# Performance work log

Measured on AMD Instinct MI355X. Metric: run time of the kernel, lower is better.

Reference implementation:

```python
import jax, jax.numpy as jnp
import numpy as np
import math

D_MODEL = 768
N_HEADS = 6
HD = D_MODEL // N_HEADS  # 128
RANK = D_MODEL // 4      # 192
B, T = 128, 256


def _rope_tables(T, dim):
    # matches torch: inv = 1/10000**(arange(0,dim,2)/dim); emb = cat([outer(t,inv)]*2, -1)
    inv = 1.0 / (10000.0 ** (jnp.arange(0, dim, 2, dtype=jnp.float32) / dim))
    t = jnp.arange(T, dtype=jnp.float32)
    freqs = jnp.outer(t, inv)                       # [T, dim/2]
    emb = jnp.concatenate([freqs, freqs], axis=-1)  # [T, dim]
    return jnp.cos(emb), jnp.sin(emb)               # each [T, dim]


def _rot(x):
    h = x.shape[-1] // 2
    return jnp.concatenate([-x[..., h:], x[..., :h]], axis=-1)


def setup_inputs() -> dict:
    key = jax.random.key(0)
    ks = jax.random.split(key, 8)
    s_in = 1.0 / math.sqrt(D_MODEL)
    s_r = 1.0 / math.sqrt(RANK)
    inp = {
        'x': jax.random.normal(ks[0], (B, T, D_MODEL), dtype=jnp.float32),
        'qA': jax.random.normal(ks[1], (D_MODEL, RANK), dtype=jnp.float32) * s_in,
        'qB': jax.random.normal(ks[2], (RANK, D_MODEL), dtype=jnp.float32) * s_r,
        'kA': jax.random.normal(ks[3], (D_MODEL, RANK), dtype=jnp.float32) * s_in,
        'kB': jax.random.normal(ks[4], (RANK, D_MODEL), dtype=jnp.float32) * s_r,
        'vA': jax.random.normal(ks[5], (D_MODEL, RANK), dtype=jnp.float32) * s_in,
        'vB': jax.random.normal(ks[6], (RANK, D_MODEL), dtype=jnp.float32) * s_r,
        'o_w': jax.random.normal(ks[7], (D_MODEL, D_MODEL), dtype=jnp.float32) * s_in,
    }
    return inp


def reference(x, qA, qB, kA, kB, vA, vB, o_w):
    Bb, Tt, _ = x.shape
    # low-rank projections: in -> rank -> out, then split heads [B, H, T, hd]
    def proj(A, W):
        h = (x @ A) @ W
        return h.reshape(Bb, Tt, N_HEADS, HD).transpose(0, 2, 1, 3)
    q = proj(qA, qB)
    k = proj(kA, kB)
    v = proj(vA, vB)
    cos, sin = _rope_tables(Tt, HD)  # [T, hd], broadcast over B, H
    q = q * cos + _rot(q) * sin
    k = k * cos + _rot(k) * sin
    att = jnp.einsum('bhqd,bhkd->bhqk', q, k) / math.sqrt(HD)
    causal = jnp.tril(jnp.ones((Tt, Tt), dtype=bool))
    att = jnp.where(causal, att, -jnp.inf)
    att = jax.nn.softmax(att, axis=-1)
    out = jnp.einsum('bhqk,bhkd->bhqd', att, v)          # [B, H, T, hd]
    out = out.transpose(0, 2, 1, 3).reshape(Bb, Tt, D_MODEL)
    return out @ o_w
```

## Files before the change

kernel.cpp:

```cpp
#include <hip/hip_runtime.h>
#include <hip/hip_bf16.h>
#include <stdint.h>

typedef __attribute__((ext_vector_type(8))) short s16x8;
typedef __attribute__((ext_vector_type(4))) float f32x4;

#define D_MODEL 768
#define N_HEADS 6
#define HD 128
#define RANK 192
#define TT 256
#define NROW 32768
#define QKV_LD 2304
#define NK 12
#define QSCL 0.08838834764831845f

__device__ inline short f2bf(float f) {
  union { float f; unsigned u; } x; x.f = f;
  unsigned r = x.u + 0x7fffu + ((x.u >> 16) & 1u);
  return (short)(r >> 16);
}
__device__ inline float bf2f(short v) {
  union { unsigned u; float f; } x; x.u = ((unsigned)(unsigned short)v) << 16;
  return x.f;
}
__device__ inline void gload_lds16(const void* g, void* lds) {
  __builtin_amdgcn_global_load_lds(
      (const __attribute__((address_space(1))) unsigned int*)g,
      (__attribute__((address_space(3))) unsigned int*)lds, 16, 0, 0);
}

#define BAR()    asm volatile("s_barrier" ::: "memory")
#define LGKM0()  asm volatile("s_waitcnt lgkmcnt(0)" ::: "memory")
#define WAITVM4() asm volatile("s_waitcnt vmcnt(4)" ::: "memory")
#define WAITVM0() asm volatile("s_waitcnt vmcnt(0)" ::: "memory")

__global__ void k_tables(float* __restrict__ cosT, float* __restrict__ sinT) {
  int tid = blockIdx.x * 256 + threadIdx.x;
  int t = tid >> 6, i = tid & 63;
  float inv = powf(10000.0f, -(float)i / 64.0f);
  float ang = (float)t * inv;
  cosT[tid] = cosf(ang);
  sinT[tid] = sinf(ang);
}

__global__ void k_castx(const float* __restrict__ x, short* __restrict__ xb) {
  int t = blockIdx.x * 256 + threadIdx.x;
  const float4* xp = (const float4*)x;
  float4 a = xp[t * 2], b = xp[t * 2 + 1];
  s16x8 o;
  o[0] = f2bf(a.x); o[1] = f2bf(a.y); o[2] = f2bf(a.z); o[3] = f2bf(a.w);
  o[4] = f2bf(b.x); o[5] = f2bf(b.y); o[6] = f2bf(b.z); o[7] = f2bf(b.w);
  *(s16x8*)(xb + (size_t)t * 8) = o;
}

__global__ void k_makew(const float* __restrict__ qA, const float* __restrict__ qB,
                        const float* __restrict__ kA, const float* __restrict__ kB,
                        const float* __restrict__ vA, const float* __restrict__ vB,
                        short* __restrict__ WT) {
  int g = blockIdx.x * 256 + threadIdx.x;
  int n4 = g % 576, kkb = g / 576;
  int part = n4 / 192, nnb = (n4 % 192) * 4;
  const float* A = (part == 0) ? qA : (part == 1) ? kA : vA;
  const float* Bm = (part == 0) ? qB : (part == 1) ? kB : vB;
  float acc[4][4] = {};
  for (int r0 = 0; r0 < RANK; r0 += 4) {
    float4 a4[4], b4[4];
#pragma unroll
    for (int q = 0; q < 4; ++q)
      a4[q] = *(const float4*)&A[(kkb + q * 192) * RANK + r0];
#pragma unroll
    for (int i = 0; i < 4; ++i)
      b4[i] = *(const float4*)&Bm[(r0 + i) * 768 + nnb];
#pragma unroll
    for (int q = 0; q < 4; ++q) {
      const float* aq = (const float*)&a4[q];
#pragma unroll
      for (int i = 0; i < 4; ++i) {
        const float* bi = (const float*)&b4[i];
#pragma unroll
        for (int jn = 0; jn < 4; ++jn)
          acc[q][jn] += aq[i] * bi[jn];
      }
    }
  }
#pragma unroll
  for (int q = 0; q < 4; ++q)
#pragma unroll
    for (int jn = 0; jn < 4; ++jn)
      WT[(size_t)(part * 768 + nnb + jn) * 768 + kkb + q * 192] = f2bf(acc[q][jn]);
}

__global__ void k_wot(const float* __restrict__ ow, short* __restrict__ WT) {
  int g = blockIdx.x * 256 + threadIdx.x;
  int n = g % 768, kk = g / 768;
  WT[(size_t)(2304 + n) * 768 + kk] = f2bf(ow[(size_t)kk * 768 + n]);
}

__device__ inline s16x8 rdfrag(const short* hbase, int rowbyte, int ksl4x, int swz) {
  return *(const s16x8*)((const char*)hbase + rowbyte + (((ksl4x) ^ (swz)) << 4));
}

template <bool OUTBF>
__global__ __launch_bounds__(512, 2) void k_gemm8(const short* __restrict__ A,
                                                  const short* __restrict__ Bt,
                                                  void* __restrict__ Cv, int ldc) {
  extern __shared__ short lds[];
  const int tid = threadIdx.x;
  const int wid = tid >> 6, lane = tid & 63;
  const int l15 = lane & 15, l4 = lane >> 4;
  const int wr = wid >> 2, wc = wid & 3;
  const int swz = l15 & 7;
  const int bid = blockIdx.y * 128 + blockIdx.x;
  const int nper = gridDim.y;
  const int xcd = bid & 7, loc = bid >> 3;
  const int mq = loc / nper;
  const int mt = xcd * 16 + mq;
  const int nt = loc - mq * nper;
  const long mbase = (long)mt * 256;
  const long nbase = (long)nt * 256;

  const int hb0 = wid * 2048 + lane * 16;
  const int hb1 = hb0 + 1024;
  const int r0 = hb0 >> 7, c0 = ((hb0 >> 4) & 7) ^ (r0 & 7);
  const int r1 = hb1 >> 7, c1 = ((hb1 >> 4) & 7) ^ (r1 & 7);
  const int off0 = r0 * 768 + c0 * 8;
  const int off1 = r1 * 768 + c1 * 8;

#define STAGE(G, rowoff, kt, ldsS) do {                                        \
    gload_lds16((G) + (size_t)(rowoff) * 768 + (kt) * 64 + off0,               \
                (char*)(ldsS) + wid * 2048);                                   \
    gload_lds16((G) + (size_t)(rowoff) * 768 + (kt) * 64 + off1,               \
                (char*)(ldsS) + wid * 2048 + 1024);                            \
  } while (0)

#define LDSA(buf, half) (lds + ((buf) * 2 + (half)) * 8192)
#define LDSB(buf, half) (lds + 32768 + ((buf) * 2 + (half)) * 8192)

  f32x4 acc[8][4] = {};

  STAGE(A,  mbase,       0, LDSA(0, 0));
  STAGE(Bt, nbase,       0, LDSB(0, 0));
  STAGE(A,  mbase + 128, 0, LDSA(0, 1));
  STAGE(Bt, nbase + 128, 0, LDSB(0, 1));
  STAGE(A,  mbase,       1, LDSA(1, 0));
  STAGE(Bt, nbase,       1, LDSB(1, 0));
  WAITVM4();
  BAR();

  s16x8 a03[4][2], a47[4][2], b01[2][2], b23[2][2];

#pragma unroll
  for (int kt = 0; kt < NK; ++kt) {
    const int buf = kt & 1, nbuf = buf ^ 1;
    const short* Ab = LDSA(buf, wr);
    const short* Bb = LDSB(buf, (wc >> 1));
    const int browbase = (wc & 1) * 64 * 128;

#pragma unroll
    for (int mf = 0; mf < 4; ++mf)
#pragma unroll
      for (int ks = 0; ks < 2; ++ks)
        a03[mf][ks] = rdfrag(Ab, (mf * 16 + l15) * 128, ks * 4 + l4, swz);
#pragma unroll
    for (int nf = 0; nf < 2; ++nf)
#pragma unroll
      for (int ks = 0; ks < 2; ++ks)
        b01[nf][ks] = rdfrag(Bb, browbase + (nf * 16 + l15) * 128, ks * 4 + l4, swz);
    if (kt + 1 < NK) STAGE(A, mbase + 128, kt + 1, LDSA(nbuf, 1));
    BAR();
    LGKM0();
    __builtin_amdgcn_s_setprio(1);
#pragma unroll
    for (int mf = 0; mf < 4; ++mf)
#pragma unroll
      for (int nf = 0; nf < 2; ++nf)
#pragma unroll
        for (int ks = 0; ks < 2; ++ks)
          acc[mf][nf] = __builtin_amdgcn_mfma_f32_16x16x32_bf16(a03[mf][ks], b01[nf][ks], acc[mf][nf], 0, 0, 0);
    __builtin_amdgcn_s_setprio(0);
    BAR();

#pragma unroll
    for (int mf = 0; mf < 4; ++mf)
#pragma unroll
      for (int ks = 0; ks < 2; ++ks)
        a47[mf][ks] = rdfrag(Ab, ((mf + 4) * 16 + l15) * 128, ks * 4 + l4, swz);
    if (kt + 1 < NK) STAGE(Bt, nbase + 128, kt + 1, LDSB(nbuf, 1));
    BAR();
    LGKM0();
    __builtin_amdgcn_s_setprio(1);
#pragma unroll
    for (int mf = 0; mf < 4; ++mf)
#pragma unroll
      for (int nf = 0; nf < 2; ++nf)
#pragma unroll
        for (int ks = 0; ks < 2; ++ks)
          acc[mf + 4][nf] = __builtin_amdgcn_mfma_f32_16x16x32_bf16(a47[mf][ks], b01[nf][ks], acc[mf + 4][nf], 0, 0, 0);
    __builtin_amdgcn_s_setprio(0);
    BAR();

#pragma unroll
    for (int nf = 0; nf < 2; ++nf)
#pragma unroll
      for (int ks = 0; ks < 2; ++ks)
        b23[nf][ks] = rdfrag(Bb, browbase + ((nf + 2) * 16 + l15) * 128, ks * 4 + l4, swz);
    if (kt + 2 < NK) STAGE(A, mbase, kt + 2, LDSA(buf, 0));
    BAR();
    LGKM0();
    __builtin_amdgcn_s_setprio(1);
#pragma unroll
    for (int mf = 0; mf < 4; ++mf)
#pragma unroll
      for (int nf = 0; nf < 2; ++nf)
#pragma unroll
        for (int ks = 0; ks < 2; ++ks)
          acc[mf][nf + 2] = __builtin_amdgcn_mfma_f32_16x16x32_bf16(a03[mf][ks], b23[nf][ks], acc[mf][nf + 2], 0, 0, 0);
    __builtin_amdgcn_s_setprio(0);
    BAR();

    if (kt + 2 < NK) STAGE(Bt, nbase, kt + 2, LDSB(buf, 0));
    BAR();
    __builtin_amdgcn_s_setprio(1);
#pragma unroll
    for (int mf = 0; mf < 4; ++mf)
#pragma unroll
      for (int nf = 0; nf < 2; ++nf)
#pragma unroll
        for (int ks = 0; ks < 2; ++ks)
          acc[mf + 4][nf + 2] = __builtin_amdgcn_mfma_f32_16x16x32_bf16(a47[mf][ks], b23[nf][ks], acc[mf + 4][nf + 2], 0, 0, 0);
    __builtin_amdgcn_s_setprio(0);
    if (kt < NK - 1) {
      if (kt + 2 < NK) WAITVM4(); else WAITVM0();
      BAR();
    }
  }
#undef STAGE

#pragma unroll
  for (int mf = 0; mf < 8; ++mf)
#pragma unroll
    for (int nf = 0; nf < 4; ++nf)
#pragma unroll
      for (int r = 0; r < 4; ++r) {
        long row = mbase + wr * 128 + mf * 16 + l4 * 4 + r;
        long col = nbase + wc * 64 + nf * 16 + l15;
        if (OUTBF) ((short*)Cv)[row * ldc + col] = f2bf(acc[mf][nf][r]);
        else       ((float*)Cv)[row * ldc + col] = acc[mf][nf][r];
      }
}

__global__ void k_ropek(short* __restrict__ qkv, const float* __restrict__ cosT,
                        const float* __restrict__ sinT) {
  int tid = blockIdx.x * 256 + threadIdx.x;
  int row = tid / 48, rem = tid % 48;
  int head = rem >> 3, i8 = (rem & 7) * 8;
  int t = row & (TT - 1);
  size_t base = (size_t)row * QKV_LD + D_MODEL + head * 128 + i8;
  s16x8 a = *(const s16x8*)(qkv + base);
  s16x8 b = *(const s16x8*)(qkv + base + 64);
  const float4* cp = (const float4*)(cosT + t * 64 + i8);
  const float4* sp = (const float4*)(sinT + t * 64 + i8);
  float4 c04 = cp[0], c14 = cp[1], s04 = sp[0], s14 = sp[1];
  float cs[8] = {c04.x, c04.y, c04.z, c04.w, c14.x, c14.y, c14.z, c14.w};
  float sn[8] = {s04.x, s04.y, s04.z, s04.w, s14.x, s14.y, s14.z, s14.w};
  s16x8 na, nb;
#pragma unroll
  for (int j = 0; j < 8; ++j) {
    float av = bf2f(a[j]), bv = bf2f(b[j]);
    na[j] = f2bf(av * cs[j] - bv * sn[j]);
    nb[j] = f2bf(bv * cs[j] + av * sn[j]);
  }
  *(s16x8*)(qkv + base) = na;
  *(s16x8*)(qkv + base + 64) = nb;
}

__global__ __launch_bounds__(512) void k_attn(const short* __restrict__ qkv,
                                              short* __restrict__ attout,
                                              const float* __restrict__ cosT,
                                              const float* __restrict__ sinT) {
  extern __shared__ short smem[];
  short* Kls0 = smem;
  short* Kls1 = smem + 8192;
  short* Vt   = smem + 16384;
  const int tid = threadIdx.x;
  const int wid = tid >> 6, lane = tid & 63;
  const int l15 = lane & 15, l4 = lane >> 4;
  short* PlsW = smem + 24576 + wid * 2048;
  const int b = blockIdx.x / N_HEADS, h = blockIdx.x % N_HEADS;
  const long row0 = (long)b * TT;
  const int d0 = wid * 16;

  s16x8 qf[2][4];
#pragma unroll
  for (int mi = 0; mi < 2; ++mi)
#pragma unroll
    for (int kc = 0; kc < 4; ++kc) {
      long row = row0 + wid * 32 + mi * 16 + l15;
      qf[mi][kc] = *(const s16x8*)(qkv + row * QKV_LD + h * HD + kc * 32 + l4 * 8);
    }
#pragma unroll
  for (int mi = 0; mi < 2; ++mi) {
    int t = wid * 32 + mi * 16 + l15;
#pragma unroll
    for (int kc = 0; kc < 2; ++kc) {
      const float4* cp = (const float4*)(cosT + t * 64 + kc * 32 + l4 * 8);
      const float4* sp = (const float4*)(sinT + t * 64 + kc * 32 + l4 * 8);
      float4 c04 = cp[0], c14 = cp[1], s04 = sp[0], s14 = sp[1];
      float cs[8] = {c04.x, c04.y, c04.z, c04.w, c14.x, c14.y, c14.z, c14.w};
      float sn[8] = {s04.x, s04.y, s04.z, s04.w, s14.x, s14.y, s14.z, s14.w};
#pragma unroll
      for (int jj = 0; jj < 8; ++jj) {
        float av = bf2f(qf[mi][kc][jj]);
        float bv = bf2f(qf[mi][kc + 2][jj]);
        qf[mi][kc][jj]     = f2bf((av * cs[jj] - bv * sn[jj]) * QSCL);
        qf[mi][kc + 2][jj] = f2bf((bv * cs[jj] + av * sn[jj]) * QSCL);
      }
    }
  }

#define STAGEK(j_, Kd) do {                                                     \
    int bb0_ = wid * 2048 + lane * 16;                                          \
    int r0_ = bb0_ >> 8; int sc0_ = ((bb0_ >> 4) & 15) ^ (r0_ & 7);             \
    gload_lds16(qkv + (row0 + (j_) * 64 + r0_) * QKV_LD + D_MODEL + h * HD + sc0_ * 8, \
                (char*)(Kd) + wid * 2048);                                      \
    int bb1_ = bb0_ + 1024;                                                     \
    int r1_ = bb1_ >> 8; int sc1_ = ((bb1_ >> 4) & 15) ^ (r1_ & 7);             \
    gload_lds16(qkv + (row0 + (j_) * 64 + r1_) * QKV_LD + D_MODEL + h * HD + sc1_ * 8, \
                (char*)(Kd) + wid * 2048 + 1024);                               \
  } while (0)

#define LOADV(j_, va, vb) do {                                                  \
    const short* vsrc_ = qkv + (row0 + (j_) * 64 + lane) * QKV_LD + 2 * D_MODEL + h * HD + d0; \
    va = *(const s16x8*)vsrc_;                                                  \
    vb = *(const s16x8*)(vsrc_ + 8);                                            \
  } while (0)

  float mst[2][4], lst[2][4];
  f32x4 oacc[2][8];
#pragma unroll
  for (int mi = 0; mi < 2; ++mi)
#pragma unroll
    for (int r = 0; r < 4; ++r) { mst[mi][r] = -1e30f; lst[mi][r] = 0.f; }
#pragma unroll
  for (int mi = 0; mi < 2; ++mi)
#pragma unroll
    for (int nd = 0; nd < 8; ++nd) oacc[mi][nd] = {0.f, 0.f, 0.f, 0.f};

  const int jmax = (wid * 32 + 31) / 64;

  STAGEK(0, Kls0);
  s16x8 vr[2][2];
  LOADV(0, vr[0][0], vr[0][1]);

#pragma unroll
  for (int j = 0; j < 4; ++j) {
    const int buf = j & 1;
    const short* Kb = buf ? Kls1 : Kls0;
    short* Kn = buf ? Kls0 : Kls1;
    if (j < 3) {
      STAGEK(j + 1, Kn);
      LOADV(j + 1, vr[buf ^ 1][0], vr[buf ^ 1][1]);
    }
    if (j < 3) WAITVM4(); else WAITVM0();
    __builtin_amdgcn_sched_barrier(0);
    BAR();
#pragma unroll
    for (int e = 0; e < 8; ++e)
      *(short*)((char*)Vt + (d0 + e) * 128 + (((lane >> 3) ^ e) << 4) + (lane & 7) * 2) = vr[buf][0][e];
#pragma unroll
    for (int e = 0; e < 8; ++e)
      *(short*)((char*)Vt + (d0 + 8 + e) * 128 + (((lane >> 3) ^ e) << 4) + (lane & 7) * 2) = vr[buf][1][e];

    if (j <= jmax) {
      f32x4 sacc[2][4] = {};
#pragma unroll
      for (int kc = 0; kc < 4; ++kc) {
        s16x8 kf[4];
#pragma unroll
        for (int ni = 0; ni < 4; ++ni)
          kf[ni] = *(const s16x8*)((const char*)Kb + (ni * 16 + l15) * 256 +
                                   (((kc * 4 + l4) ^ (l15 & 7)) << 4));
#pragma unroll
        for (int mi = 0; mi < 2; ++mi)
#pragma unroll
          for (int ni = 0; ni < 4; ++ni)
            sacc[mi][ni] = __builtin_amdgcn_mfma_f32_16x16x32_bf16(qf[mi][kc], kf[ni], sacc[mi][ni], 0, 0, 0);
      }
#pragma unroll
      for (int mi = 0; mi < 2; ++mi) {
#pragma unroll
        for (int r = 0; r < 4; ++r) {
          int qr = wid * 32 + mi * 16 + l4 * 4 + r;
          float rm = -1e30f;
#pragma unroll
          for (int ni = 0; ni < 4; ++ni) {
            int kvc = j * 64 + ni * 16 + l15;
            if (kvc > qr) sacc[mi][ni][r] = -1e30f;
            rm = fmaxf(rm, sacc[mi][ni][r]);
          }
#pragma unroll
          for (int d2 = 1; d2 < 16; d2 <<= 1)
            rm = fmaxf(rm, __shfl_xor(rm, d2, 64));
          float mold = mst[mi][r];
          float mnew = fmaxf(mold, rm);
          float alpha = __expf(mold - mnew);
          mst[mi][r] = mnew;
          float rs = 0.f;
#pragma unroll
          for (int ni = 0; ni < 4; ++ni) {
            float p = __expf(sacc[mi][ni][r] - mnew);
            sacc[mi][ni][r] = p;
            rs += p;
          }
#pragma unroll
          for (int d2 = 1; d2 < 16; d2 <<= 1)
            rs += __shfl_xor(rs, d2, 64);
          lst[mi][r] = lst[mi][r] * alpha + rs;
#pragma unroll
          for (int nd = 0; nd < 8; ++nd)
            oacc[mi][nd][r] *= alpha;
        }
      }
#pragma unroll
      for (int mi = 0; mi < 2; ++mi)
#pragma unroll
        for (int ni = 0; ni < 4; ++ni)
#pragma unroll
          for (int r = 0; r < 4; ++r) {
            int prow = mi * 16 + l4 * 4 + r;
            int pcp = (ni * 2 + (l15 >> 3)) ^ (prow & 7);
            *(short*)((char*)PlsW + prow * 128 + (pcp << 4) + (l15 & 7) * 2) =
                f2bf(sacc[mi][ni][r]);
          }
    }
    LGKM0();
    BAR();
    __builtin_amdgcn_sched_barrier(0);
    if (j <= jmax) {
#pragma unroll
      for (int kc2 = 0; kc2 < 2; ++kc2) {
        s16x8 pa[2];
#pragma unroll
        for (int mi = 0; mi < 2; ++mi)
          pa[mi] = *(const s16x8*)((const char*)PlsW + (mi * 16 + l15) * 128 +
                                   (((kc2 * 4 + l4) ^ (l15 & 7)) << 4));
#pragma unroll
        for (int nd = 0; nd < 8; ++nd) {
          s16x8 vf = *(const s16x8*)((const char*)Vt + (nd * 16 + l15) * 128 +
                                     (((kc2 * 4 + l4) ^ (l15 & 7)) << 4));
#pragma unroll
          for (int mi = 0; mi < 2; ++mi)
            oacc[mi][nd] = __builtin_amdgcn_mfma_f32_16x16x32_bf16(pa[mi], vf, oacc[mi][nd], 0, 0, 0);
        }
      }
    }
  }
#undef STAGEK
#undef LOADV
#pragma unroll
  for (int mi = 0; mi < 2; ++mi)
#pragma unroll
    for (int nd = 0; nd < 8; ++nd)
#pragma unroll
      for (int r = 0; r < 4; ++r) {
        long row = row0 + wid * 32 + mi * 16 + l4 * 4 + r;
        int col = h * HD + nd * 16 + l15;
        attout[row * D_MODEL + col] = f2bf(oacc[mi][nd][r] / lst[mi][r]);
      }
}

extern "C" void kernel_launch(void* const* d_in, const int* in_sizes, int n_in,
                              void* d_out, int out_size, void* d_ws, size_t ws_size,
                              hipStream_t stream) {
  const float* x  = (const float*)d_in[0];
  const float* qA = (const float*)d_in[1];
  const float* qB = (const float*)d_in[2];
  const float* kA = (const float*)d_in[3];
  const float* kB = (const float*)d_in[4];
  const float* vA = (const float*)d_in[5];
  const float* vB = (const float*)d_in[6];
  const float* ow = (const float*)d_in[7];

  char* ws = (char*)d_ws;
  short* qkv   = (short*)ws;
  short* xb    = (short*)(ws + 150994944);
  short* WT    = (short*)(ws + 201326592);
  float* cosT  = (float*)(ws + 206045184);
  float* sinT  = (float*)(ws + 206110720);
  short* attout = xb;

  hipFuncSetAttribute((const void*)k_gemm8<true>,
                      hipFuncAttributeMaxDynamicSharedMemorySize, 131072);
  hipFuncSetAttribute((const void*)k_gemm8<false>,
                      hipFuncAttributeMaxDynamicSharedMemorySize, 131072);
  hipFuncSetAttribute((const void*)k_attn,
                      hipFuncAttributeMaxDynamicSharedMemorySize, 81920);

  k_tables<<<64, 256, 0, stream>>>(cosT, sinT);
  k_castx<<<12288, 256, 0, stream>>>(x, xb);
  k_makew<<<432, 256, 0, stream>>>(qA, qB, kA, kB, vA, vB, WT);
  k_wot<<<2304, 256, 0, stream>>>(ow, WT);
  k_gemm8<true><<<dim3(128, 9), 512, 131072, stream>>>(xb, WT, (void*)qkv, QKV_LD);
  k_ropek<<<6144, 256, 0, stream>>>(qkv, cosT, sinT);
  k_attn<<<768, 512, 81920, stream>>>(qkv, attout, cosT, sinT);
  k_gemm8<false><<<dim3(128, 3), 512, 131072, stream>>>(attout, WT + (size_t)2304 * 768, d_out, 768);
}
```

Measured before the change: 362.2 us.

## Store Q/K/V in head-major [B,H,T,hd] layout from the projection GEMM epilogue

Result: faster. 353.8 us (median of 2 runs) (-2.3%).

```diff
diff --git a/kernel.cpp b/kernel.cpp
--- a/kernel.cpp
+++ b/kernel.cpp
@@ -11,9 +11,9 @@
 #define RANK 192
 #define TT 256
 #define NROW 32768
-#define QKV_LD 2304
 #define NK 12
 #define QSCL 0.08838834764831845f
+#define PSTRIDE 25165824
 
 __device__ inline short f2bf(float f) {
   union { float f; unsigned u; } x; x.f = f;
@@ -101,7 +101,7 @@
   return *(const s16x8*)((const char*)hbase + rowbyte + (((ksl4x) ^ (swz)) << 4));
 }
 
-template <bool OUTBF>
+template <int MODE>
 __global__ __launch_bounds__(512, 2) void k_gemm8(const short* __restrict__ A,
                                                   const short* __restrict__ Bt,
                                                   void* __restrict__ Cv, int ldc) {
@@ -240,25 +240,33 @@
 #pragma unroll
   for (int mf = 0; mf < 8; ++mf)
 #pragma unroll
-    for (int nf = 0; nf < 4; ++nf)
+    for (int nf = 0; nf < 4; ++nf) {
+      const int col = (int)(nbase + wc * 64 + nf * 16 + l15);
+      const int part = col / 768;
+      const int wi = col - part * 768;
+      const int hh = wi >> 7, dd = wi & 127;
 #pragma unroll
       for (int r = 0; r < 4; ++r) {
         long row = mbase + wr * 128 + mf * 16 + l4 * 4 + r;
-        long col = nbase + wc * 64 + nf * 16 + l15;
-        if (OUTBF) ((short*)Cv)[row * ldc + col] = f2bf(acc[mf][nf][r]);
-        else       ((float*)Cv)[row * ldc + col] = acc[mf][nf][r];
-      }
-}
-
-__global__ void k_ropek(short* __restrict__ qkv, const float* __restrict__ cosT,
+        if (MODE == 0) {
+          ((float*)Cv)[row * ldc + col] = acc[mf][nf][r];
+        } else {
+          size_t idx = (size_t)part * PSTRIDE +
+                       (((size_t)(row >> 8) * 6 + hh) * 256 + (row & 255)) * 128 + dd;
+          ((short*)Cv)[idx] = f2bf(acc[mf][nf][r]);
+        }
+      }
+    }
+}
+
+__global__ void k_ropek(short* __restrict__ kp, const float* __restrict__ cosT,
                         const float* __restrict__ sinT) {
   int tid = blockIdx.x * 256 + threadIdx.x;
-  int row = tid / 48, rem = tid % 48;
-  int head = rem >> 3, i8 = (rem & 7) * 8;
-  int t = row & (TT - 1);
-  size_t base = (size_t)row * QKV_LD + D_MODEL + head * 128 + i8;
-  s16x8 a = *(const s16x8*)(qkv + base);
-  s16x8 b = *(const s16x8*)(qkv + base + 64);
+  int bh = tid >> 11, rem = tid & 2047;
+  int t = rem >> 3, i8 = (rem & 7) * 8;
+  size_t base = ((size_t)bh * 256 + t) * 128 + i8;
+  s16x8 a = *(const s16x8*)(kp + base);
+  s16x8 b = *(const s16x8*)(kp + base + 64);
   const float4* cp = (const float4*)(cosT + t * 64 + i8);
   const float4* sp = (const float4*)(sinT + t * 64 + i8);
   float4 c04 = cp[0], c14 = cp[1], s04 = sp[0], s14 = sp[1];
@@ -271,11 +279,13 @@
     na[j] = f2bf(av * cs[j] - bv * sn[j]);
     nb[j] = f2bf(bv * cs[j] + av * sn[j]);
   }
-  *(s16x8*)(qkv + base) = na;
-  *(s16x8*)(qkv + base + 64) = nb;
-}
-
-__global__ __launch_bounds__(512) void k_attn(const short* __restrict__ qkv,
+  *(s16x8*)(kp + base) = na;
+  *(s16x8*)(kp + base + 64) = nb;
+}
+
+__global__ __launch_bounds__(512) void k_attn(const short* __restrict__ qp,
+                                              const short* __restrict__ kp,
+                                              const short* __restrict__ vp,
                                               short* __restrict__ attout,
                                               const float* __restrict__ cosT,
                                               const float* __restrict__ sinT) {
@@ -287,8 +297,10 @@
   const int wid = tid >> 6, lane = tid & 63;
   const int l15 = lane & 15, l4 = lane >> 4;
   short* PlsW = smem + 24576 + wid * 2048;
-  const int b = blockIdx.x / N_HEADS, h = blockIdx.x % N_HEADS;
+  const int bh = blockIdx.x;
+  const int b = bh / N_HEADS, h = bh % N_HEADS;
   const long row0 = (long)b * TT;
+  const size_t pbase = (size_t)bh * 256 * 128;
   const int d0 = wid * 16;
 
   s16x8 qf[2][4];
@@ -296,8 +308,8 @@
   for (int mi = 0; mi < 2; ++mi)
 #pragma unroll
     for (int kc = 0; kc < 4; ++kc) {
-      long row = row0 + wid * 32 + mi * 16 + l15;
-      qf[mi][kc] = *(const s16x8*)(qkv + row * QKV_LD + h * HD + kc * 32 + l4 * 8);
+      int t = wid * 32 + mi * 16 + l15;
+      qf[mi][kc] = *(const s16x8*)(qp + pbase + (size_t)t * 128 + kc * 32 + l4 * 8);
     }
 #pragma unroll
   for (int mi = 0; mi < 2; ++mi) {
@@ -322,16 +334,16 @@
 #define STAGEK(j_, Kd) do {                                                     \
     int bb0_ = wid * 2048 + lane * 16;                                          \
     int r0_ = bb0_ >> 8; int sc0_ = ((bb0_ >> 4) & 15) ^ (r0_ & 7);             \
-    gload_lds16(qkv + (row0 + (j_) * 64 + r0_) * QKV_LD + D_MODEL + h * HD + sc0_ * 8, \
+    gload_lds16(kp + pbase + (size_t)((j_) * 64 + r0_) * 128 + sc0_ * 8,        \
                 (char*)(Kd) + wid * 2048);                                      \
     int bb1_ = bb0_ + 1024;                                                     \
     int r1_ = bb1_ >> 8; int sc1_ = ((bb1_ >> 4) & 15) ^ (r1_ & 7);             \
-    gload_lds16(qkv + (row0 + (j_) * 64 + r1_) * QKV_LD + D_MODEL + h * HD + sc1_ * 8, \
+    gload_lds16(kp + pbase + (size_t)((j_) * 64 + r1_) * 128 + sc1_ * 8,        \
                 (char*)(Kd) + wid * 2048 + 1024);                               \
   } while (0)
 
 #define LOADV(j_, va, vb) do {                                                  \
-    const short* vsrc_ = qkv + (row0 + (j_) * 64 + lane) * QKV_LD + 2 * D_MODEL + h * HD + d0; \
+    const short* vsrc_ = vp + pbase + (size_t)((j_) * 64 + lane) * 128 + d0;    \
     va = *(const s16x8*)vsrc_;                                                  \
     vb = *(const s16x8*)(vsrc_ + 8);                                            \
   } while (0)
@@ -483,16 +495,19 @@
   const float* ow = (const float*)d_in[7];
 
   char* ws = (char*)d_ws;
-  short* qkv   = (short*)ws;
+  short* qkvp  = (short*)ws;
+  short* qp    = qkvp;
+  short* kp    = qkvp + (size_t)PSTRIDE;
+  short* vp    = qkvp + (size_t)2 * PSTRIDE;
   short* xb    = (short*)(ws + 150994944);
   short* WT    = (short*)(ws + 201326592);
   float* cosT  = (float*)(ws + 206045184);
   float* sinT  = (float*)(ws + 206110720);
   short* attout = xb;
 
-  hipFuncSetAttribute((const void*)k_gemm8<true>,
+  hipFuncSetAttribute((const void*)k_gemm8<2>,
                       hipFuncAttributeMaxDynamicSharedMemorySize, 131072);
-  hipFuncSetAttribute((const void*)k_gemm8<false>,
+  hipFuncSetAttribute((const void*)k_gemm8<0>,
                       hipFuncAttributeMaxDynamicSharedMemorySize, 131072);
   hipFuncSetAttribute((const void*)k_attn,
                       hipFuncAttributeMaxDynamicSharedMemorySize, 81920);
@@ -501,8 +516,8 @@
   k_castx<<<12288, 256, 0, stream>>>(x, xb);
   k_makew<<<432, 256, 0, stream>>>(qA, qB, kA, kB, vA, vB, WT);
   k_wot<<<2304, 256, 0, stream>>>(ow, WT);
-  k_gemm8<true><<<dim3(128, 9), 512, 131072, stream>>>(xb, WT, (void*)qkv, QKV_LD);
-  k_ropek<<<6144, 256, 0, stream>>>(qkv, cosT, sinT);
-  k_attn<<<768, 512, 81920, stream>>>(qkv, attout, cosT, sinT);
-  k_gemm8<false><<<dim3(128, 3), 512, 131072, stream>>>(attout, WT + (size_t)2304 * 768, d_out, 768);
-}
+  k_gemm8<2><<<dim3(128, 9), 512, 131072, stream>>>(xb, WT, (void*)qkvp, 0);
+  k_ropek<<<6144, 256, 0, stream>>>(kp, cosT, sinT);
+  k_attn<<<768, 512, 81920, stream>>>(qp, kp, vp, attout, cosT, sinT);
+  k_gemm8<0><<<dim3(128, 3), 512, 131072, stream>>>(attout, WT + (size_t)2304 * 768, d_out, 768);
+}
```
